# Performance work log

Measured on AMD Instinct MI355X. Metric: run time of the kernel, lower is better.

Reference implementation:

```python
import jax, jax.numpy as jnp
import numpy as np

REFSIZE = 1024  # init kwarg refsize -> self.N
EPS = float(np.finfo(np.float32).eps)


def interp1d(x, y, xnew):
    """Batched linear interpolation, faithful to Interp1d.forward.
    x, y: (D, N) with x sorted along last dim; xnew: (D, P). Returns (D, P)."""
    # torch.searchsorted default (right=False) == numpy/jnp side='left'
    ind = jax.vmap(jnp.searchsorted)(x, xnew) - 1
    ind = jnp.clip(ind, 0, x.shape[1] - 2)
    slopes = (y[:, 1:] - y[:, :-1]) / (EPS + (x[:, 1:] - x[:, :-1]))
    x_sel = jnp.take_along_axis(x, ind, axis=1)
    y_sel = jnp.take_along_axis(y, ind, axis=1)
    s_sel = jnp.take_along_axis(slopes, ind, axis=1)
    return y_sel + s_sel * (xnew - x_sel)


def setup_inputs() -> dict:
    key = jax.random.key(0)
    k1, k2 = jax.random.split(key)
    l, n = 2048, 4096
    x1 = jax.random.uniform(k1, (l, n), dtype=jnp.float32)  # points on [0,1)
    w = jax.random.uniform(k2, (l, n), dtype=jnp.float32)
    x1_weights = w / jnp.sum(w, axis=-1, keepdims=True)  # row-normalized masses
    return {"x1": x1, "x1_weights": x1_weights}


def reference(x1, x1_weights):
    l, n = x1.shape
    N = REFSIZE
    ref = jnp.linspace(0.0, 1.0, N + 1, dtype=jnp.float32)[:-1]  # (N,)

    # empirical_cdf: sort samples, cumsum weights
    order = jnp.argsort(x1, axis=-1)
    xs = jnp.take_along_axis(x1, order, axis=-1)          # (l, n) sorted samples
    ys = jnp.cumsum(jnp.take_along_axis(x1_weights, order, axis=-1), axis=-1)  # CDF

    # emb
    alpha = (jnp.sum(x1 * x1_weights, axis=-1) / jnp.sum(x1_weights, axis=-1) - 0.5)[:, None]
    xnew = jnp.broadcast_to(jnp.linspace(-1.0, 2.0, 3 * N, dtype=jnp.float32)[None, :], (l, 3 * N))
    int_x = jnp.floor(xnew)
    rest_x = xnew - int_x
    ecdf = int_x + interp1d(xs, ys, rest_x)               # (l, 3N) extended CDF

    x_grid = jnp.broadcast_to(ref[None, :], (l, N))
    embedd = interp1d(ecdf, xnew, x_grid - alpha) - x_grid  # inverse-CDF embedding

    # circular cost
    a = jnp.abs(embedd)
    m = jnp.minimum(a, 1.0 - a)
    return jnp.sqrt(jnp.mean(jnp.sum(m * m, axis=-1)) + 1e-8)
```

## Files before the change

kernel.cpp:

```cpp
#include <hip/hip_runtime.h>
#include <math.h>

#define L    2048
#define NCOL 4096
#define NG   1024
#define N3   3072
#define T    512
#define NW   8
#define EPT  8
#define NB   3072
#define NBW  1536
#define FEPS 1.1920929e-07f

typedef unsigned long long u64;
typedef unsigned short u16;
typedef unsigned int u32;

__device__ __forceinline__ int lower_bound_f(const float* a, int lo, int hi, float v) {
  while (lo < hi) {
    int mid = (lo + hi) >> 1;
    if (a[mid] < v) lo = mid + 1; else hi = mid;
  }
  return lo;
}

__device__ __forceinline__ int bucket_of_bits(unsigned xb) {
  float f = __uint_as_float(xb);
  int b = (int)(f * (float)NB);
  return b > NB - 1 ? NB - 1 : b;
}

__device__ __forceinline__ int swz(int i) { return i ^ ((i >> 5) & 7); }

__global__ __launch_bounds__(T, 8) void lcot_rows(const float* __restrict__ X,
                                                  const float* __restrict__ W,
                                                  float* __restrict__ rowsum,
                                                  u32* __restrict__ done_cnt,
                                                  float* __restrict__ out) {
  extern __shared__ char smem[];
  u64*   pairs = (u64*)smem;
  float* xs    = (float*)smem;
  float* wy    = (float*)(smem + 16384);
  float* ecdf  = (float*)(smem + 16384);
  u16*   cnt16 = (u16*)(smem + 32768);
  u32*   cntw  = (u32*)(smem + 32768);

  __shared__ float redA[NW], redB[NW], fwt[NW];
  __shared__ int   iwt[NW];
  __shared__ float s_alpha;
  __shared__ int   s_last;

  const int tid  = threadIdx.x;
  const int lane = tid & 63;
  const int wave = tid >> 6;
  const int row  = blockIdx.x;
  const float* xr = X + (size_t)row * NCOL;
  const float* wr = W + (size_t)row * NCOL;

  for (int i = tid; i < NBW + 1; i += T) cntw[i] = 0u;

  u64 key[EPT];
  float sxw = 0.f, sw = 0.f;
  const float4* xr4 = (const float4*)xr;
  const float4* wr4 = (const float4*)wr;
#pragma unroll
  for (int c = 0; c < 2; ++c) {
    float4 xv = xr4[tid * 2 + c];
    float4 ww = wr4[tid * 2 + c];
    sxw += xv.x * ww.x + xv.y * ww.y + xv.z * ww.z + xv.w * ww.w;
    sw  += ww.x + ww.y + ww.z + ww.w;
    int b = 8 * tid + 4 * c;
    key[4*c+0] = ((u64)__float_as_uint(xv.x) << 32) | (unsigned)(b + 0);
    key[4*c+1] = ((u64)__float_as_uint(xv.y) << 32) | (unsigned)(b + 1);
    key[4*c+2] = ((u64)__float_as_uint(xv.z) << 32) | (unsigned)(b + 2);
    key[4*c+3] = ((u64)__float_as_uint(xv.w) << 32) | (unsigned)(b + 3);
  }
#pragma unroll
  for (int off = 32; off > 0; off >>= 1) {
    sxw += __shfl_down(sxw, off);
    sw  += __shfl_down(sw, off);
  }
  if (lane == 0) { redA[wave] = sxw; redB[wave] = sw; }
  __syncthreads();

  u32 bo[EPT];
#pragma unroll
  for (int e = 0; e < EPT; ++e) {
    int b = bucket_of_bits((unsigned)(key[e] >> 32));
    u32 inc = (b & 1) ? 65536u : 1u;
    u32 ret = atomicAdd(&cntw[b >> 1], inc);
    u32 o = (b & 1) ? (ret >> 16) : (ret & 0xffffu);
    bo[e] = ((u32)b << 16) | (o & 0xffffu);
  }
  __syncthreads();
  if (tid == 0) {
    float a = 0.f, b = 0.f;
#pragma unroll
    for (int i = 0; i < NW; ++i) { a += redA[i]; b += redB[i]; }
    s_alpha = a / b - 0.5f;
  }

  u32 cv0 = cntw[3 * tid], cv1 = cntw[3 * tid + 1], cv2 = cntw[3 * tid + 2];
  int c0 = (int)(cv0 & 0xffffu), c1 = (int)(cv0 >> 16);
  int c2 = (int)(cv1 & 0xffffu), c3 = (int)(cv1 >> 16);
  int c4 = (int)(cv2 & 0xffffu), c5 = (int)(cv2 >> 16);
  int runi = c0 + c1 + c2 + c3 + c4 + c5;
  int toti = runi, prei = runi;
#pragma unroll
  for (int off = 1; off < 64; off <<= 1) {
    int v = __shfl_up(prei, off);
    if (lane >= off) prei += v;
  }
  if (lane == 63) iwt[wave] = prei;
  __syncthreads();
  int wpre = 0;
#pragma unroll
  for (int w2 = 0; w2 < NW; ++w2) wpre += (w2 < wave) ? iwt[w2] : 0;
  int acc = wpre + prei - toti;
  {
    int b0 = acc; acc += c0;
    int b1 = acc; acc += c1;
    int b2 = acc; acc += c2;
    int b3 = acc; acc += c3;
    int b4 = acc; acc += c4;
    int b5 = acc; acc += c5;
    cntw[3 * tid]     = (u32)b0 | ((u32)b1 << 16);
    cntw[3 * tid + 1] = (u32)b2 | ((u32)b3 << 16);
    cntw[3 * tid + 2] = (u32)b4 | ((u32)b5 << 16);
  }
  if (tid == T - 1) cnt16[NB] = (u16)acc;
  __syncthreads();

#pragma unroll
  for (int e = 0; e < EPT; ++e) {
    int b = (int)(bo[e] >> 16);
    int o = (int)(bo[e] & 0xffffu);
    pairs[(int)cnt16[b] + o] = key[e];
  }
  __syncthreads();

#pragma unroll
  for (int bb = 0; bb < 6; ++bb) {
    int b  = 6 * tid + bb;
    int lo = (int)cnt16[b], hi = (int)cnt16[b + 1];
    int n = hi - lo;
    if (n >= 2) {
      int hm1 = hi - 1;
      u64 e0 = pairs[lo];
      u64 e1 = pairs[lo + 1];
      u64 t2 = pairs[lo + 2 < hm1 ? lo + 2 : hm1];
      u64 t3 = pairs[lo + 3 < hm1 ? lo + 3 : hm1];
      u64 e2 = (n > 2) ? t2 : ~0ull;
      u64 e3 = (n > 3) ? t3 : ~0ull;
      { u64 a = e0 < e1 ? e0 : e1; e1 = e0 < e1 ? e1 : e0; e0 = a; }
      { u64 a = e2 < e3 ? e2 : e3; e3 = e2 < e3 ? e3 : e2; e2 = a; }
      { u64 a = e0 < e2 ? e0 : e2; e2 = e0 < e2 ? e2 : e0; e0 = a; }
      { u64 a = e1 < e3 ? e1 : e3; e3 = e1 < e3 ? e3 : e1; e1 = a; }
      { u64 a = e1 < e2 ? e1 : e2; e2 = e1 < e2 ? e2 : e1; e1 = a; }
      pairs[lo]     = e0;
      pairs[lo + 1] = e1;
      if (n > 2) pairs[lo + 2] = e2;
      if (n > 3) pairs[lo + 3] = e3;
      for (int i2 = lo + 4; i2 < hi; ++i2) {
        u64 v = pairs[i2];
        int j = i2 - 1;
        while (j >= lo && pairs[j] > v) { pairs[j + 1] = pairs[j]; --j; }
        pairs[j + 1] = v;
      }
    }
  }
  __syncthreads();

  u64 q[EPT];
#pragma unroll
  for (int m = 0; m < EPT; ++m) q[m] = pairs[tid + m * T];
  float wg[EPT];
#pragma unroll
  for (int m = 0; m < EPT; ++m) wg[m] = wr[(u32)(q[m] & 0xffffffffu)];
  __syncthreads();

#pragma unroll
  for (int m = 0; m < EPT; ++m) {
    int j = tid + m * T;
    xs[j]      = __uint_as_float((u32)(q[m] >> 32));
    wy[swz(j)] = wg[m];
  }
  __syncthreads();

  float lw[EPT];
  float runf = 0.f;
#pragma unroll
  for (int c = 0; c < EPT; ++c) {
    runf += wy[swz(8 * tid + c)];
    lw[c] = runf;
  }
  float totf = runf, pref = runf;
#pragma unroll
  for (int off = 1; off < 64; off <<= 1) {
    float v = __shfl_up(pref, off);
    if (lane >= off) pref += v;
  }
  if (lane == 63) fwt[wave] = pref;
  __syncthreads();
  float wpf = 0.f;
#pragma unroll
  for (int w2 = 0; w2 < NW; ++w2) wpf += (w2 < wave) ? fwt[w2] : 0.f;
  float basef = wpf + pref - totf;
#pragma unroll
  for (int c = 0; c < EPT; ++c) wy[swz(8 * tid + c)] = basef + lw[c];
  __syncthreads();

  float ev[N3 / T];
#pragma unroll
  for (int g = 0; g < 2; ++g) {
    int lo0, hi0, lo1, hi1, lo2, hi2;
    float r0, r1, r2;
    {
      int j = tid + (3 * g + 0) * T;
      float xnew = -1.0f + (3.0f * (float)j) / 3071.0f;
      r0 = xnew - floorf(xnew);
      int k = (int)(r0 * (float)NB); k = k > NB - 1 ? NB - 1 : k;
      lo0 = (int)cnt16[k]; hi0 = (int)cnt16[k + 1];
    }
    {
      int j = tid + (3 * g + 1) * T;
      float xnew = -1.0f + (3.0f * (float)j) / 3071.0f;
      r1 = xnew - floorf(xnew);
      int k = (int)(r1 * (float)NB); k = k > NB - 1 ? NB - 1 : k;
      lo1 = (int)cnt16[k]; hi1 = (int)cnt16[k + 1];
    }
    {
      int j = tid + (3 * g + 2) * T;
      float xnew = -1.0f + (3.0f * (float)j) / 3071.0f;
      r2 = xnew - floorf(xnew);
      int k = (int)(r2 * (float)NB); k = k > NB - 1 ? NB - 1 : k;
      lo2 = (int)cnt16[k]; hi2 = (int)cnt16[k + 1];
    }
    while ((lo0 < hi0) | (lo1 < hi1) | (lo2 < hi2)) {
      if (lo0 < hi0) { int m = (lo0 + hi0) >> 1; if (xs[m] < r0) lo0 = m + 1; else hi0 = m; }
      if (lo1 < hi1) { int m = (lo1 + hi1) >> 1; if (xs[m] < r1) lo1 = m + 1; else hi1 = m; }
      if (lo2 < hi2) { int m = (lo2 + hi2) >> 1; if (xs[m] < r2) lo2 = m + 1; else hi2 = m; }
    }
#pragma unroll
    for (int s3 = 0; s3 < 3; ++s3) {
      int s = 3 * g + s3;
      int lb = (s3 == 0) ? lo0 : (s3 == 1) ? lo1 : lo2;
      float rest = (s3 == 0) ? r0 : (s3 == 1) ? r1 : r2;
      int j = tid + s * T;
      float xnew = -1.0f + (3.0f * (float)j) / 3071.0f;
      float ix = floorf(xnew);
      int ind = lb - 1;
      ind = ind < 0 ? 0 : (ind > NCOL - 2 ? NCOL - 2 : ind);
      float x0 = xs[ind], x1v = xs[ind + 1];
      float y0 = wy[swz(ind)], y1v = wy[swz(ind + 1)];
      float slope = (y1v - y0) * __builtin_amdgcn_rcpf(FEPS + (x1v - x0));
      ev[s] = ix + (y0 + slope * (rest - x0));
    }
  }
  __syncthreads();

#pragma unroll
  for (int s = 0; s < N3 / T; ++s) ecdf[tid + s * T] = ev[s];
  __syncthreads();

  float alpha = s_alpha;
  float accf = 0.f;
  {
    float xg0 = (float)tid / 1024.0f;
    float xg1 = (float)(tid + T) / 1024.0f;
    float q0 = xg0 - alpha;
    float q1 = xg1 - alpha;
    int lo0 = 0, hi0 = N3, lo1 = 0, hi1 = N3;
    while ((lo0 < hi0) | (lo1 < hi1)) {
      if (lo0 < hi0) { int m = (lo0 + hi0) >> 1; if (ecdf[m] < q0) lo0 = m + 1; else hi0 = m; }
      if (lo1 < hi1) { int m = (lo1 + hi1) >> 1; if (ecdf[m] < q1) lo1 = m + 1; else hi1 = m; }
    }
#pragma unroll
    for (int s = 0; s < 2; ++s) {
      int lo = (s == 0) ? lo0 : lo1;
      float q2 = (s == 0) ? q0 : q1;
      float xg = (s == 0) ? xg0 : xg1;
      int ind = lo - 1;
      ind = ind < 0 ? 0 : (ind > N3 - 2 ? N3 - 2 : ind);
      float e0 = ecdf[ind], e1 = ecdf[ind + 1];
      float y0 = -1.0f + (3.0f * (float)ind) / 3071.0f;
      float y1 = -1.0f + (3.0f * (float)(ind + 1)) / 3071.0f;
      float slope = (y1 - y0) * __builtin_amdgcn_rcpf(FEPS + (e1 - e0));
      float emb = y0 + slope * (q2 - e0) - xg;
      float a = fabsf(emb);
      float m = fminf(a, 1.0f - a);
      accf += m * m;
    }
  }
#pragma unroll
  for (int off = 32; off > 0; off >>= 1) accf += __shfl_down(accf, off);
  if (lane == 0) redA[wave] = accf;
  __syncthreads();

  if (tid == 0) {
    float s = 0.f;
#pragma unroll
    for (int i = 0; i < NW; ++i) s += redA[i];
    __hip_atomic_store(&rowsum[row], s, __ATOMIC_RELEASE, __HIP_MEMORY_SCOPE_AGENT);
    u32 old = __hip_atomic_fetch_add(done_cnt, 1u, __ATOMIC_ACQ_REL,
                                     __HIP_MEMORY_SCOPE_AGENT);
    s_last = (old == (u32)(L - 1));
  }
  __syncthreads();
  if (s_last) {
    float s = 0.f;
    if (tid < 256) {
      for (int i = tid; i < L; i += 256)
        s += __hip_atomic_load(&rowsum[i], __ATOMIC_RELAXED, __HIP_MEMORY_SCOPE_AGENT);
#pragma unroll
      for (int off = 32; off > 0; off >>= 1) s += __shfl_down(s, off);
      if ((tid & 63) == 0) redB[tid >> 6] = s;
    }
    __syncthreads();
    if (tid == 0) {
      float tot = redB[0] + redB[1] + redB[2] + redB[3];
      out[0] = sqrtf(tot / (float)L + 1e-8f);
    }
  }
}

extern "C" void kernel_launch(void* const* d_in, const int* in_sizes, int n_in,
                              void* d_out, int out_size, void* d_ws, size_t ws_size,
                              hipStream_t stream) {
  const float* X = (const float*)d_in[0];
  const float* W = (const float*)d_in[1];
  float* rowsum = (float*)d_ws;
  u32*   done   = (u32*)((char*)d_ws + L * sizeof(float));
  hipMemsetAsync(done, 0, sizeof(u32), stream);
  size_t shbytes = 32768 + 6152;
  hipLaunchKernelGGL(lcot_rows, dim3(L), dim3(T), shbytes, stream,
                     X, W, rowsum, done, (float*)d_out);
}
```

Measured before the change: 175.5 us.

## Store CDF in place inside sorted key/index pairs, dropping separate xs/wy arrays

After sorting, each thread now reads its 8 contiguous pairs with vector loads, gathers the weights and scans them directly from registers. The cumulative weights are written back into the low word of each pair, so the sorted x and the CDF value sit together in one 64-bit entry. This removes a staging pass through separate xs/wy shared arrays, one barrier and the swizzle. Interpolation then needs a single 64-bit LDS load per point, while binary search reads 32-bit words at a stride of two. The strided 32-bit writes of the CDF may cause LDS bank conflicts.

```diff
diff --git a/kernel.cpp b/kernel.cpp
--- a/kernel.cpp
+++ b/kernel.cpp
@@ -30,8 +30,6 @@
   return b > NB - 1 ? NB - 1 : b;
 }
 
-__device__ __forceinline__ int swz(int i) { return i ^ ((i >> 5) & 7); }
-
 __global__ __launch_bounds__(T, 8) void lcot_rows(const float* __restrict__ X,
                                                   const float* __restrict__ W,
                                                   float* __restrict__ rowsum,
@@ -39,9 +37,8 @@
                                                   float* __restrict__ out) {
   extern __shared__ char smem[];
   u64*   pairs = (u64*)smem;
-  float* xs    = (float*)smem;
-  float* wy    = (float*)(smem + 16384);
-  float* ecdf  = (float*)(smem + 16384);
+  u32*   pw    = (u32*)smem;
+  float* ecdf  = (float*)smem;
   u16*   cnt16 = (u16*)(smem + 32768);
   u32*   cntw  = (u32*)(smem + 32768);
 
@@ -172,28 +169,18 @@
   __syncthreads();
 
   u64 q[EPT];
-#pragma unroll
-  for (int m = 0; m < EPT; ++m) q[m] = pairs[tid + m * T];
+  {
+    const ulonglong2* pr2 = (const ulonglong2*)pairs + 4 * tid;
+#pragma unroll
+    for (int c = 0; c < 4; ++c) { ulonglong2 v = pr2[c]; q[2*c] = v.x; q[2*c+1] = v.y; }
+  }
   float wg[EPT];
 #pragma unroll
-  for (int m = 0; m < EPT; ++m) wg[m] = wr[(u32)(q[m] & 0xffffffffu)];
-  __syncthreads();
-
-#pragma unroll
-  for (int m = 0; m < EPT; ++m) {
-    int j = tid + m * T;
-    xs[j]      = __uint_as_float((u32)(q[m] >> 32));
-    wy[swz(j)] = wg[m];
-  }
-  __syncthreads();
-
+  for (int e = 0; e < EPT; ++e) wg[e] = wr[(u32)(q[e] & 0xffffffffu)];
   float lw[EPT];
   float runf = 0.f;
 #pragma unroll
-  for (int c = 0; c < EPT; ++c) {
-    runf += wy[swz(8 * tid + c)];
-    lw[c] = runf;
-  }
+  for (int c = 0; c < EPT; ++c) { runf += wg[c]; lw[c] = runf; }
   float totf = runf, pref = runf;
 #pragma unroll
   for (int off = 1; off < 64; off <<= 1) {
@@ -207,7 +194,8 @@
   for (int w2 = 0; w2 < NW; ++w2) wpf += (w2 < wave) ? fwt[w2] : 0.f;
   float basef = wpf + pref - totf;
 #pragma unroll
-  for (int c = 0; c < EPT; ++c) wy[swz(8 * tid + c)] = basef + lw[c];
+  for (int c = 0; c < EPT; ++c)
+    pw[2 * (8 * tid + c)] = __float_as_uint(basef + lw[c]);
   __syncthreads();
 
   float ev[N3 / T];
@@ -237,9 +225,12 @@
       lo2 = (int)cnt16[k]; hi2 = (int)cnt16[k + 1];
     }
     while ((lo0 < hi0) | (lo1 < hi1) | (lo2 < hi2)) {
-      if (lo0 < hi0) { int m = (lo0 + hi0) >> 1; if (xs[m] < r0) lo0 = m + 1; else hi0 = m; }
-      if (lo1 < hi1) { int m = (lo1 + hi1) >> 1; if (xs[m] < r1) lo1 = m + 1; else hi1 = m; }
-      if (lo2 < hi2) { int m = (lo2 + hi2) >> 1; if (xs[m] < r2) lo2 = m + 1; else hi2 = m; }
+      if (lo0 < hi0) { int m = (lo0 + hi0) >> 1;
+        if (__uint_as_float(pw[2 * m + 1]) < r0) lo0 = m + 1; else hi0 = m; }
+      if (lo1 < hi1) { int m = (lo1 + hi1) >> 1;
+        if (__uint_as_float(pw[2 * m + 1]) < r1) lo1 = m + 1; else hi1 = m; }
+      if (lo2 < hi2) { int m = (lo2 + hi2) >> 1;
+        if (__uint_as_float(pw[2 * m + 1]) < r2) lo2 = m + 1; else hi2 = m; }
     }
 #pragma unroll
     for (int s3 = 0; s3 < 3; ++s3) {
@@ -251,8 +242,12 @@
       float ix = floorf(xnew);
       int ind = lb - 1;
       ind = ind < 0 ? 0 : (ind > NCOL - 2 ? NCOL - 2 : ind);
-      float x0 = xs[ind], x1v = xs[ind + 1];
-      float y0 = wy[swz(ind)], y1v = wy[swz(ind + 1)];
+      u64 v0 = pairs[ind];
+      u64 v1 = pairs[ind + 1];
+      float x0  = __uint_as_float((u32)(v0 >> 32));
+      float y0  = __uint_as_float((u32)(v0 & 0xffffffffu));
+      float x1v = __uint_as_float((u32)(v1 >> 32));
+      float y1v = __uint_as_float((u32)(v1 & 0xffffffffu));
       float slope = (y1v - y0) * __builtin_amdgcn_rcpf(FEPS + (x1v - x0));
       ev[s] = ix + (y0 + slope * (rest - x0));
     }
```

After: 183.9 us. +4.8%, slower.
